# Optimization experiments

Hardware: AMD Instinct MI355X
Metric: run time of the kernel (lower is better)

Reference implementation:

```python
import jax, jax.numpy as jnp
import numpy as np
from jax import lax

# Static module config (init_kwargs), classic FlowNetC correlation settings
K = 1      # kernel_size (odd)
MD = 20    # max_displacement
S1 = 1     # stride1 (output stride over data1 centers)
S2 = 2     # stride2 (displacement grid stride)
PAD = 20   # pad_size


def _corr(data1, data2, scale1, scale2, out_scale):
    """FlowNet-style multiplicative correlation cost volume.

    data1, data2: [B, C, H, W] (dequantized-domain float values).
    Returns [B, D*D, outH, outW] with D = 2*MD//S2 + 1.
    Math matches the quantized op with rounding omitted: the int accumulator
    acc = sum_{c,k} q1*q2 is rescaled by scale1*scale2, averaged over
    sumelems = K*K*C, and requantized by dividing by out_scale.
    """
    B, C, H, W = data1.shape
    Hp, Wp = H + 2 * PAD, W + 2 * PAD
    D = 2 * MD // S2 + 1
    p1 = jnp.pad(data1, ((0, 0), (0, 0), (PAD, PAD), (PAD, PAD)))
    # pad data2 by an extra MD so every displacement is a static slice
    p2 = jnp.pad(data2, ((0, 0), (0, 0), (PAD + MD, PAD + MD), (PAD + MD, PAD + MD)))
    maps = []
    for i in range(D):          # fixed small displacement grid (21x21)
        for j in range(D):
            sh = p2[:, :, i * S2:i * S2 + Hp, j * S2:j * S2 + Wp]
            maps.append(jnp.einsum('bchw,bchw->bhw', p1, sh))  # channel reduction
    cm = jnp.stack(maps, axis=1)  # [B, D*D, Hp, Wp]
    # valid output centers start at border = MD + (K-1)//2; window start = border - r = MD
    cm = cm[:, :, MD:Hp - MD, MD:Wp - MD]
    if K > 1 or S1 > 1:
        cm = lax.reduce_window(cm, jnp.float32(0.0), lax.add,
                               (1, 1, K, K), (1, 1, S1, S1), 'VALID')
    sumelems = K * K * C
    return cm * (scale1[0] * scale2[0]) / (sumelems * out_scale[0])


def setup_inputs() -> dict:
    key = jax.random.key(0)
    k1, k2 = jax.random.split(key)
    B, C, H, W = 8, 96, 64, 96
    data1 = jax.random.normal(k1, (B, C, H, W), dtype=jnp.float32)
    data2 = jax.random.normal(k2, (B, C, H, W), dtype=jnp.float32)
    return {
        'data1': data1,
        'data2': data2,
        'scale1': jnp.ones((1,), jnp.float32),
        'scale2': jnp.ones((1,), jnp.float32),
        'inter_scale': jnp.ones((1,), jnp.float32),
        'out_scale': jnp.ones((1,), jnp.float32),
    }


def reference(data1, data2, scale1, scale2, inter_scale, out_scale):
    # inter_scale only affects integer rounding in the quantized op; with
    # rounding omitted it is an identity rescale (requant then dequant).
    return _corr(data1, data2, scale1, scale2, out_scale)
```

## Files before the change

### kernel.cpp

```cpp
#include <hip/hip_runtime.h>
#include <hip/hip_bf16.h>

#define B_ 8
#define C_ 96
#define H_ 64
#define W_ 96
#define DD 21
#define NI 3
#define ISPLIT 7
#define LDSTm 37
#define RAWS 49

typedef __attribute__((ext_vector_type(8))) short sh8;
typedef __attribute__((ext_vector_type(4))) float fx4;

__device__ __attribute__((aligned(16))) unsigned short g_d1F[B_*H_*2*3*3*512];
__device__ __attribute__((aligned(16))) unsigned short g_d2F[(size_t)B_*64*2*5*3*512];

__global__ __launch_bounds__(256) void prep_all(const float* __restrict__ d1,
                                                const float* __restrict__ d2) {
  __shared__ unsigned int raw[C_*RAWS];
  const int b = blockIdx.x & 7;
  const int t = blockIdx.x >> 3;

  if (t >= 64) {
    const int y = t - 64;
    unsigned short* ob = g_d2F + (size_t)(b*64 + y)*(2*15*512);
    for (int idx = threadIdx.x; idx < C_*48; idx += 256) {
      int c = idx / 48, w = idx % 48;
      const float2 v = *(const float2*)(d2 + (((b*C_ + c)*H_ + y)*W_ + 2*w));
      __hip_bfloat16 h0 = __float2bfloat16(v.x), h1 = __float2bfloat16(v.y);
      raw[c*RAWS + w] = (unsigned)*(unsigned short*)&h0 |
                        ((unsigned)*(unsigned short*)&h1 << 16);
    }
    __syncthreads();
    for (int s = threadIdx.x; s < 2*15*64; s += 256) {
      int lane = s & 63, q = s >> 6;
      int kk = q % 3, wt = (q/3) % 5, p = q / 15;
      int w = wt*16 + (lane & 15) - 10;
      int cb = kk*32 + (lane >> 4)*8;
      uint4 o; o.x = o.y = o.z = o.w = 0u;
      if (w >= 0 && w < 48) {
        unsigned short tmp[8];
        #pragma unroll
        for (int e = 0; e < 8; ++e) {
          unsigned pk = raw[(cb + e)*RAWS + w];
          tmp[e] = (unsigned short)(p ? (pk >> 16) : pk);
        }
        o = *(const uint4*)tmp;
      }
      *(uint4*)(ob + (size_t)s*8) = o;
    }
  } else {
    const int y = t;
    for (int idx = threadIdx.x; idx < C_*48; idx += 256) {
      int c = idx / 48, w = idx % 48;
      const float2 v = *(const float2*)(d1 + (((b*C_ + c)*H_ + y)*W_ + 2*w));
      __hip_bfloat16 h0 = __float2bfloat16(v.x), h1 = __float2bfloat16(v.y);
      raw[c*RAWS + w] = (unsigned)*(unsigned short*)&h0 |
                        ((unsigned)*(unsigned short*)&h1 << 16);
    }
    __syncthreads();
    unsigned short* ob = g_d1F + (size_t)(b*H_ + y)*(2*9*512);
    for (int s = threadIdx.x; s < 2*9*64; s += 256) {
      int lane = s & 63, q = s >> 6;
      int kk = q % 3, ut = (q/3) % 3, p = q / 9;
      int w = ut*16 + (lane & 15);
      int cb = kk*32 + (lane >> 4)*8;
      unsigned short tmp[8];
      #pragma unroll
      for (int e = 0; e < 8; ++e) {
        unsigned pk = raw[(cb + e)*RAWS + w];
        tmp[e] = (unsigned short)(p ? (pk >> 16) : pk);
      }
      *(uint4*)(ob + (size_t)s*8) = *(const uint4*)tmp;
    }
  }
}

#define SYNC_LDS asm volatile("s_waitcnt lgkmcnt(0)\n\ts_barrier" ::: "memory")

#define LOADB(BF, ROW) do {                                                    \
    const int row_ = (ROW);                                                    \
    if (row_ >= 20 && row_ < 84) {                                             \
      const unsigned short* rb_ =                                              \
          g_d2F + (size_t)(((b*64 + (row_ - 20))*2 + p)*5 + mt)*(3*512)        \
          + lane*8;                                                            \
      _Pragma("unroll")                                                        \
      for (int n_ = 0; n_ < 3; ++n_)                                           \
        _Pragma("unroll")                                                      \
        for (int k_ = 0; k_ < 3; ++k_)                                         \
          BF[k_*3+n_] = *(const sh8*)(rb_ + (n_*3 + k_)*512);                  \
    } else {                                                                   \
      _Pragma("unroll")                                                        \
      for (int t_ = 0; t_ < 9; ++t_)                                           \
        BF[t_] = (sh8){0,0,0,0,0,0,0,0};                                       \
    }                                                                          \
  } while (0)

#define COMBO(BF, I, BUF) do {                                                 \
    fx4 acc[3] = {fx4{0,0,0,0}, fx4{0,0,0,0}, fx4{0,0,0,0}};                   \
    _Pragma("unroll")                                                          \
    for (int k_ = 0; k_ < 3; ++k_)                                             \
      _Pragma("unroll")                                                        \
      for (int n_ = 0; n_ < 3; ++n_)                                           \
        acc[n_] = __builtin_amdgcn_mfma_f32_16x16x32_bf16(aF[k_], BF[k_*3+n_], \
                                                          acc[n_], 0, 0, 0);   \
    _Pragma("unroll")                                                          \
    for (int n_ = 0; n_ < 3; ++n_)                                             \
      _Pragma("unroll")                                                        \
      for (int r_ = 0; r_ < 4; ++r_) {                                         \
        int j_ = 16*n_ + lr - 4*lg - r_;                                       \
        if (j_ >= 0 && j_ < DD)                                                \
          Dst[BUF][j_*LDSTm + 2*(4*lg + r_) + p] = acc[n_][r_];                \
      }                                                                        \
    SYNC_LDS;                                                                  \
    size_t obase = (size_t)((b*441 + (I)*DD)*H_ + y)*W_ + 2*m0;                \
    for (int q_ = threadIdx.x; q_ < DD*8; q_ += 128) {                         \
      int j_ = q_ >> 3, xi_ = q_ & 7;                                          \
      const float* rp_ = &Dst[BUF][j_*LDSTm + xi_*4];                          \
      fx4 v_; v_[0] = rp_[0]; v_[1] = rp_[1]; v_[2] = rp_[2]; v_[3] = rp_[3];  \
      v_ = v_ * scale;                                                         \
      __builtin_nontemporal_store(                                             \
          v_, (fx4*)(out + obase + (size_t)j_*(H_*W_) + xi_*4));               \
    }                                                                          \
  } while (0)

__global__ __launch_bounds__(128, 4) void corr_main(const float* __restrict__ s1,
                                                    const float* __restrict__ s2,
                                                    const float* __restrict__ os,
                                                    float* __restrict__ out) {
  __shared__ float Dst[2][DD*LDSTm];
  const int gid = blockIdx.x;
  const int b = gid & 7;
  int t = gid >> 3;
  const int mt = t % 3; t /= 3;
  const int m0 = mt << 4;
  const int y = t & 63;
  const int i0 = (t >> 6) * NI;
  const int p = threadIdx.x >> 6;
  const int lane = threadIdx.x & 63;
  const int lr = lane & 15, lg = lane >> 4;
  const float scale = s1[0]*s2[0] / (96.0f * os[0]);

  sh8 aF[3];
  {
    const unsigned short* aB =
        g_d1F + (size_t)((b*H_ + y)*2 + p)*(9*512) + (size_t)mt*3*512 + lane*8;
    #pragma unroll
    for (int k = 0; k < 3; ++k)
      aF[k] = *(const sh8*)(aB + k*512);
  }

  sh8 bF0[9], bF1[9];
  const int yb = y + 2*i0;
  LOADB(bF0, yb);
  LOADB(bF1, yb + 2);
  COMBO(bF0, i0,     0);
  LOADB(bF0, yb + 4);
  COMBO(bF1, i0 + 1, 1);
  COMBO(bF0, i0 + 2, 0);
}

extern "C" void kernel_launch(void* const* d_in, const int* in_sizes, int n_in,
                              void* d_out, int out_size, void* d_ws, size_t ws_size,
                              hipStream_t stream) {
  const float* d1 = (const float*)d_in[0];
  const float* d2 = (const float*)d_in[1];
  const float* s1 = (const float*)d_in[2];
  const float* s2 = (const float*)d_in[3];
  const float* os = (const float*)d_in[5];

  prep_all<<<128*B_, 256, 0, stream>>>(d1, d2);
  corr_main<<<B_*3*H_*ISPLIT, 128, 0, stream>>>(s1, s2, os, (float*)d_out);
}
```

Baseline: 42.23 us.

## Share data2 row loads across two output rows per block, longer displacement chunks

Each block now handles two output rows (y0 and y0+2). Because displacement row i for row y+2 reads the same data2 row as displacement i+1 for row y, each loaded B fragment feeds two MFMA combos, roughly halving global B loads. Displacement chunks grow from 3 to 7 and the grid shrinks accordingly, with a triple-buffered LDS staging area and full __syncthreads in place of the custom barrier. The cost is fewer blocks, so less parallelism, plus more registers and more LDS per block.

```diff
diff --git a/kernel.cpp b/kernel.cpp
--- a/kernel.cpp
+++ b/kernel.cpp
@@ -6,8 +6,8 @@
 #define H_ 64
 #define W_ 96
 #define DD 21
-#define NI 3
-#define ISPLIT 7
+#define NI 7
+#define ISPLIT 3
 #define LDSTm 37
 #define RAWS 49
 
@@ -78,8 +78,6 @@
   }
 }
 
-#define SYNC_LDS asm volatile("s_waitcnt lgkmcnt(0)\n\ts_barrier" ::: "memory")
-
 #define LOADB(BF, ROW) do {                                                    \
     const int row_ = (ROW);                                                    \
     if (row_ >= 20 && row_ < 84) {                                             \
@@ -98,13 +96,13 @@
     }                                                                          \
   } while (0)
 
-#define COMBO(BF, I, BUF) do {                                                 \
+#define COMBO(AF, Y, I, BUF) do {                                              \
     fx4 acc[3] = {fx4{0,0,0,0}, fx4{0,0,0,0}, fx4{0,0,0,0}};                   \
     _Pragma("unroll")                                                          \
     for (int k_ = 0; k_ < 3; ++k_)                                             \
       _Pragma("unroll")                                                        \
       for (int n_ = 0; n_ < 3; ++n_)                                           \
-        acc[n_] = __builtin_amdgcn_mfma_f32_16x16x32_bf16(aF[k_], BF[k_*3+n_], \
+        acc[n_] = __builtin_amdgcn_mfma_f32_16x16x32_bf16(AF[k_], bF[k_*3+n_], \
                                                           acc[n_], 0, 0, 0);   \
     _Pragma("unroll")                                                          \
     for (int n_ = 0; n_ < 3; ++n_)                                             \
@@ -114,8 +112,8 @@
         if (j_ >= 0 && j_ < DD)                                                \
           Dst[BUF][j_*LDSTm + 2*(4*lg + r_) + p] = acc[n_][r_];                \
       }                                                                        \
-    SYNC_LDS;                                                                  \
-    size_t obase = (size_t)((b*441 + (I)*DD)*H_ + y)*W_ + 2*m0;                \
+    __syncthreads();                                                           \
+    size_t obase = (size_t)((b*441 + (I)*DD)*H_ + (Y))*W_ + 2*m0;              \
     for (int q_ = threadIdx.x; q_ < DD*8; q_ += 128) {                         \
       int j_ = q_ >> 3, xi_ = q_ & 7;                                          \
       const float* rp_ = &Dst[BUF][j_*LDSTm + xi_*4];                          \
@@ -130,36 +128,45 @@
                                                     const float* __restrict__ s2,
                                                     const float* __restrict__ os,
                                                     float* __restrict__ out) {
-  __shared__ float Dst[2][DD*LDSTm];
+  __shared__ float Dst[3][DD*LDSTm];
   const int gid = blockIdx.x;
   const int b = gid & 7;
   int t = gid >> 3;
   const int mt = t % 3; t /= 3;
   const int m0 = mt << 4;
-  const int y = t & 63;
-  const int i0 = (t >> 6) * NI;
+  const int g = t & 31;
+  const int i0 = (t >> 5) * NI;
+  const int y0 = (g >> 1)*4 + (g & 1);
   const int p = threadIdx.x >> 6;
   const int lane = threadIdx.x & 63;
   const int lr = lane & 15, lg = lane >> 4;
   const float scale = s1[0]*s2[0] / (96.0f * os[0]);
 
-  sh8 aF[3];
+  sh8 aF0[3], aF1[3];
   {
-    const unsigned short* aB =
-        g_d1F + (size_t)((b*H_ + y)*2 + p)*(9*512) + (size_t)mt*3*512 + lane*8;
+    const unsigned short* a0 =
+        g_d1F + (size_t)((b*H_ + y0)*2 + p)*(9*512) + (size_t)mt*3*512 + lane*8;
+    const unsigned short* a1 =
+        g_d1F + (size_t)((b*H_ + y0 + 2)*2 + p)*(9*512) + (size_t)mt*3*512 + lane*8;
     #pragma unroll
-    for (int k = 0; k < 3; ++k)
-      aF[k] = *(const sh8*)(aB + k*512);
+    for (int k = 0; k < 3; ++k) {
+      aF0[k] = *(const sh8*)(a0 + k*512);
+      aF1[k] = *(const sh8*)(a1 + k*512);
+    }
   }
 
-  sh8 bF0[9], bF1[9];
-  const int yb = y + 2*i0;
-  LOADB(bF0, yb);
-  LOADB(bF1, yb + 2);
-  COMBO(bF0, i0,     0);
-  LOADB(bF0, yb + 4);
-  COMBO(bF1, i0 + 1, 1);
-  COMBO(bF0, i0 + 2, 0);
+  sh8 bF[9];
+  const int r0 = y0 + 2*i0;
+  LOADB(bF, r0);
+  COMBO(aF0, y0, i0, 0);
+  #pragma unroll
+  for (int d = 1; d < NI; ++d) {
+    LOADB(bF, r0 + 2*d);
+    COMBO(aF0, y0,     i0 + d,     (2*d - 1) % 3);
+    COMBO(aF1, y0 + 2, i0 + d - 1, (2*d) % 3);
+  }
+  LOADB(bF, r0 + 2*NI);
+  COMBO(aF1, y0 + 2, i0 + NI - 1, (2*NI - 1) % 3);
 }
 
 extern "C" void kernel_launch(void* const* d_in, const int* in_sizes, int n_in,
@@ -172,5 +179,5 @@
   const float* os = (const float*)d_in[5];
 
   prep_all<<<128*B_, 256, 0, stream>>>(d1, d2);
-  corr_main<<<B_*3*H_*ISPLIT, 128, 0, stream>>>(s1, s2, os, (float*)d_out);
+  corr_main<<<B_*3*32*ISPLIT, 128, 0, stream>>>(s1, s2, os, (float*)d_out);
 }
```

New measurement: 39.38 us (median of 2 runs). 6.8% less time.
